# Kernel tuning notes

Measured on AMD Instinct MI355X. Metric: run time of the kernel, lower is better.

## Reference

```python
import jax, jax.numpy as jnp
import numpy as np

N = 12288
F_DIM = 512
H1 = 32
H2 = 16
E_RAND = N * 32  # 393216 random edges; self-loops appended (DGL graph built from adj + I)


def setup_inputs() -> dict:
    key = jax.random.key(0)
    ks = jax.random.split(key, 8)
    feat = jax.random.normal(ks[0], (N, F_DIM), dtype=jnp.float32)
    src_r = jax.random.randint(ks[1], (E_RAND,), 0, N, dtype=jnp.int32)
    dst_r = jax.random.randint(ks[2], (E_RAND,), 0, N, dtype=jnp.int32)
    loop = jnp.arange(N, dtype=jnp.int32)
    src = jnp.concatenate([src_r, loop])  # [E_RAND + N]
    dst = jnp.concatenate([dst_r, loop])
    s1 = 1.0 / np.sqrt(F_DIM)
    s2 = 1.0 / np.sqrt(H1)
    W1 = jax.random.normal(ks[3], (F_DIM, H1), dtype=jnp.float32) * s1
    W2 = jax.random.normal(ks[4], (H1, H2), dtype=jnp.float32) * s2
    W3 = jax.random.normal(ks[5], (H1, H2), dtype=jnp.float32) * s2
    b1 = jnp.zeros((H1,), jnp.float32)
    b2 = jnp.zeros((H2,), jnp.float32)
    b3 = jnp.zeros((H2,), jnp.float32)
    return {"feat": feat, "src": src, "dst": dst,
            "W1": W1, "b1": b1, "W2": W2, "b2": b2, "W3": W3, "b3": b3}


def _norms(src, dst):
    ones = jnp.ones(src.shape[0], jnp.float32)
    deg_out = jax.ops.segment_sum(ones, src, num_segments=N)
    deg_in = jax.ops.segment_sum(ones, dst, num_segments=N)
    inv_sqrt_out = jnp.where(deg_out > 0, jax.lax.rsqrt(jnp.maximum(deg_out, 1.0)), 0.0)
    inv_sqrt_in = jnp.where(deg_in > 0, jax.lax.rsqrt(jnp.maximum(deg_in, 1.0)), 0.0)
    return inv_sqrt_out, inv_sqrt_in


def _graph_conv(x, src, dst, n_src, n_dst, W, b):
    # DGL GraphConv, norm='both': D_in^{-1/2} * A_agg( D_out^{-1/2} * x ) @ W + b
    # (project first when in_dim > out_dim is math-equivalent; do agg-then-W here)
    xn = x * n_src[:, None]
    msg = xn[src]  # gather along edges  [E, d]
    agg = jax.ops.segment_sum(msg, dst, num_segments=N)  # scatter-add SpMM
    h = agg * n_dst[:, None]
    return h @ W + b


def reference(feat, src, dst, W1, b1, W2, b2, W3, b3):
    n_src, n_dst = _norms(src, dst)
    h1 = jax.nn.relu(_graph_conv(feat, src, dst, n_src, n_dst, W1, b1))
    mu = _graph_conv(h1, src, dst, n_src, n_dst, W2, b2)
    logvar = _graph_conv(h1, src, dst, n_src, n_dst, W3, b3)
    # eval-mode reparameterize -> z = mu; InnerProductDecoder with identity act
    z = mu
    adj_rec = z @ z.T  # [N, N] logits
    return adj_rec, mu, logvar
```

## Files before the change

kernel.cpp:

```cpp
#include <hip/hip_runtime.h>
#include <cstddef>

#define NN 12288
#define FD 512
#define H1 32
#define H2 16

typedef float floatx4 __attribute__((ext_vector_type(4)));
typedef float floatx2 __attribute__((ext_vector_type(2)));

__global__ __launch_bounds__(256) void k_gemm1(const float* __restrict__ feat,
                                               const float* __restrict__ W1,
                                               float* __restrict__ P,
                                               int* __restrict__ degz) {
    int gz = blockIdx.x * 256 + threadIdx.x;
    if (gz < 2 * NN) degz[gz] = 0;

    __shared__ float Wlds[FD * H1];
    int tid = threadIdx.x;
    for (int t = tid; t < FD * H1 / 4; t += 256) {
        ((float4*)Wlds)[t] = ((const float4*)W1)[t];
    }
    __syncthreads();

    int row = blockIdx.x * 64 + (tid >> 2);
    int cg  = (tid & 3) * 8;
    float acc[8] = {};
    const float4* f4 = (const float4*)(feat + (size_t)row * FD);
#pragma unroll 4
    for (int k4 = 0; k4 < FD / 4; ++k4) {
        float4 f = f4[k4];
        const float* w = &Wlds[(k4 * 4) * H1 + cg];
#pragma unroll
        for (int j = 0; j < 8; ++j) {
            acc[j] += f.x * w[j] + f.y * w[H1 + j] + f.z * w[2 * H1 + j] + f.w * w[3 * H1 + j];
        }
    }
#pragma unroll
    for (int j = 0; j < 8; ++j) P[(size_t)row * H1 + cg + j] = acc[j];
}

__global__ void k_degree(const int* __restrict__ src, const int* __restrict__ dst,
                         int* __restrict__ deg_out, int* __restrict__ deg_in, int E) {
    int e = blockIdx.x * 256 + threadIdx.x;
    if (e < E) {
        atomicAdd(&deg_out[src[e]], 1);
        atomicAdd(&deg_in[dst[e]], 1);
    }
}

__global__ __launch_bounds__(1024) void k_scan(int* __restrict__ deg_out_cnt,
                                               const int* __restrict__ deg_in,
                                               int* __restrict__ row_ptr,
                                               float* __restrict__ n_src,
                                               float* __restrict__ n_dst) {
    __shared__ int wsum[16];
    int tid = threadIdx.x;
    const int CH = NN / 1024;
    int base = tid * CH;
    int v[CH];
#pragma unroll
    for (int t = 0; t < CH; ++t) v[t] = deg_in[base + t];
    int s = 0;
#pragma unroll
    for (int t = 0; t < CH; ++t) { int x = v[t]; v[t] = s; s += x; }
    int lane = tid & 63;
    int incl = s;
#pragma unroll
    for (int off = 1; off < 64; off <<= 1) {
        int up = __shfl_up(incl, off);
        if (lane >= off) incl += up;
    }
    int wid = tid >> 6;
    if (lane == 63) wsum[wid] = incl;
    __syncthreads();
    if (tid == 0) {
        int a = 0;
        for (int w = 0; w < 16; ++w) { int x = wsum[w]; wsum[w] = a; a += x; }
    }
    __syncthreads();
    int excl = incl - s + wsum[wid];
#pragma unroll
    for (int t = 0; t < CH; ++t) row_ptr[base + t] = excl + v[t];
    if (tid == 1023) row_ptr[NN] = excl + s;

#pragma unroll
    for (int t = 0; t < CH; ++t) {
        int i = base + t;
        n_src[i] = rsqrtf((float)deg_out_cnt[i]);
        n_dst[i] = rsqrtf((float)deg_in[i]);
        deg_out_cnt[i] = 0;
    }
}

__global__ void k_scatter(const int* __restrict__ src, const int* __restrict__ dst,
                          const int* __restrict__ row_ptr, int* __restrict__ cnt,
                          int* __restrict__ sorted_src, int E) {
    int e = blockIdx.x * 256 + threadIdx.x;
    if (e < E) {
        int d = dst[e];
        int pos = row_ptr[d] + atomicAdd(&cnt[d], 1);
        sorted_src[pos] = src[e];
    }
}

__global__ __launch_bounds__(256) void k_agg1(const int* __restrict__ row_ptr,
                                              const int* __restrict__ sorted_src,
                                              const float* __restrict__ P,
                                              const float* __restrict__ n_src,
                                              const float* __restrict__ n_dst,
                                              const float* __restrict__ b1,
                                              float* __restrict__ h1s) {
    int r = blockIdx.x * 8 + (threadIdx.x >> 5);
    int j = threadIdx.x & 31;
    int beg = row_ptr[r], end = row_ptr[r + 1];
    float s = 0.0f;
    int e = beg;
    for (; e + 3 < end; e += 4) {
        int s0 = sorted_src[e], s1 = sorted_src[e + 1];
        int s2 = sorted_src[e + 2], s3 = sorted_src[e + 3];
        float w0 = n_src[s0], w1 = n_src[s1], w2 = n_src[s2], w3 = n_src[s3];
        s += w0 * P[(size_t)s0 * H1 + j] + w1 * P[(size_t)s1 * H1 + j]
           + w2 * P[(size_t)s2 * H1 + j] + w3 * P[(size_t)s3 * H1 + j];
    }
    for (; e < end; ++e) {
        int s0 = sorted_src[e];
        s += n_src[s0] * P[(size_t)s0 * H1 + j];
    }
    float h = fmaxf(s * n_dst[r] + b1[j], 0.0f);
    h1s[(size_t)r * H1 + j] = h * n_src[r];
}

__global__ __launch_bounds__(256) void k_agg2(const int* __restrict__ row_ptr,
                                              const int* __restrict__ sorted_src,
                                              const float* __restrict__ h1s,
                                              const float* __restrict__ n_dst,
                                              const float* __restrict__ W2, const float* __restrict__ b2,
                                              const float* __restrict__ W3, const float* __restrict__ b3,
                                              float* __restrict__ mu, float* __restrict__ lv) {
    __shared__ float W2l[H1 * H2], W3l[H1 * H2];
    __shared__ float S[8][H1];
    int tid = threadIdx.x;
    for (int t = tid; t < H1 * H2; t += 256) { W2l[t] = W2[t]; W3l[t] = W3[t]; }

    int r0 = blockIdx.x * 8;
    int rl = tid >> 5, j = tid & 31;
    int r = r0 + rl;
    int beg = row_ptr[r], end = row_ptr[r + 1];
    float s = 0.0f;
    int e = beg;
    for (; e + 3 < end; e += 4) {
        int s0 = sorted_src[e], s1 = sorted_src[e + 1];
        int s2 = sorted_src[e + 2], s3 = sorted_src[e + 3];
        s += h1s[(size_t)s0 * H1 + j] + h1s[(size_t)s1 * H1 + j]
           + h1s[(size_t)s2 * H1 + j] + h1s[(size_t)s3 * H1 + j];
    }
    for (; e < end; ++e) s += h1s[(size_t)sorted_src[e] * H1 + j];
    S[rl][j] = s * n_dst[r];
    __syncthreads();

    int rr = tid >> 5;
    int c = tid & 15;
    bool is_lv = (tid & 16) != 0;
    const float* W = is_lv ? W3l : W2l;
    float acc = is_lv ? b3[c] : b2[c];
#pragma unroll
    for (int k = 0; k < H1; ++k) acc += S[rr][k] * W[k * H2 + c];
    float* o = is_lv ? lv : mu;
    o[(size_t)(r0 + rr) * H2 + c] = acc;
}

#define TILE 128
__global__ __launch_bounds__(256) void k_adj(const float* __restrict__ mu, float* __restrict__ out) {
    __shared__ float Alt[H2][TILE];
    __shared__ float Blt[H2][TILE];
    int tid = threadIdx.x;
    int i0 = blockIdx.y * TILE;
    int j0 = blockIdx.x * TILE;

    {
        int row = tid >> 1;
        int h8  = (tid & 1) * 8;
        float4 a0 = *(const float4*)&mu[(size_t)(i0 + row) * H2 + h8];
        float4 a1 = *(const float4*)&mu[(size_t)(i0 + row) * H2 + h8 + 4];
        Alt[h8 + 0][row] = a0.x; Alt[h8 + 1][row] = a0.y; Alt[h8 + 2][row] = a0.z; Alt[h8 + 3][row] = a0.w;
        Alt[h8 + 4][row] = a1.x; Alt[h8 + 5][row] = a1.y; Alt[h8 + 6][row] = a1.z; Alt[h8 + 7][row] = a1.w;
        float4 b0 = *(const float4*)&mu[(size_t)(j0 + row) * H2 + h8];
        float4 b1 = *(const float4*)&mu[(size_t)(j0 + row) * H2 + h8 + 4];
        Blt[h8 + 0][row] = b0.x; Blt[h8 + 1][row] = b0.y; Blt[h8 + 2][row] = b0.z; Blt[h8 + 3][row] = b0.w;
        Blt[h8 + 4][row] = b1.x; Blt[h8 + 5][row] = b1.y; Blt[h8 + 6][row] = b1.z; Blt[h8 + 7][row] = b1.w;
    }
    __syncthreads();

    int tx = tid & 15;
    int ty = tid >> 4;
    floatx2 acc2[8][4] = {};
#pragma unroll 2
    for (int k = 0; k < H2; ++k) {
        floatx4 a0 = *(const floatx4*)&Alt[k][ty * 8];
        floatx4 a1 = *(const floatx4*)&Alt[k][ty * 8 + 4];
        floatx4 b0 = *(const floatx4*)&Blt[k][tx * 8];
        floatx4 b1 = *(const floatx4*)&Blt[k][tx * 8 + 4];
        float a[8] = {a0.x, a0.y, a0.z, a0.w, a1.x, a1.y, a1.z, a1.w};
        floatx2 bp[4];
        bp[0] = (floatx2){b0.x, b0.y}; bp[1] = (floatx2){b0.z, b0.w};
        bp[2] = (floatx2){b1.x, b1.y}; bp[3] = (floatx2){b1.z, b1.w};
#pragma unroll
        for (int ii = 0; ii < 8; ++ii) {
            floatx2 av = (floatx2){a[ii], a[ii]};
#pragma unroll
            for (int jp = 0; jp < 4; ++jp)
                acc2[ii][jp] = __builtin_elementwise_fma(av, bp[jp], acc2[ii][jp]);
        }
    }

#pragma unroll
    for (int ii = 0; ii < 8; ++ii) {
        size_t row = (size_t)(i0 + ty * 8 + ii);
        float4 v0 = make_float4(acc2[ii][0].x, acc2[ii][0].y, acc2[ii][1].x, acc2[ii][1].y);
        float4 v1 = make_float4(acc2[ii][2].x, acc2[ii][2].y, acc2[ii][3].x, acc2[ii][3].y);
        *(float4*)&out[row * NN + j0 + tx * 8 + 0] = v0;
        *(float4*)&out[row * NN + j0 + tx * 8 + 4] = v1;
    }
}

extern "C" void kernel_launch(void* const* d_in, const int* in_sizes, int n_in,
                              void* d_out, int out_size, void* d_ws, size_t ws_size,
                              hipStream_t stream) {
    const float* feat = (const float*)d_in[0];
    const int*   src  = (const int*)d_in[1];
    const int*   dst  = (const int*)d_in[2];
    const float* W1   = (const float*)d_in[3];
    const float* b1   = (const float*)d_in[4];
    const float* W2   = (const float*)d_in[5];
    const float* b2   = (const float*)d_in[6];
    const float* W3   = (const float*)d_in[7];
    const float* b3   = (const float*)d_in[8];
    int E = in_sizes[1];

    int* iws = (int*)d_ws;
    int* deg_out_cnt = iws;
    int* deg_in      = iws + NN;
    int* row_ptr     = iws + 2 * NN;
    int* sorted_src  = iws + 3 * NN + 64;
    float* fws   = (float*)(iws + 3 * NN + 64 + E);
    float* n_src = fws;
    float* n_dst = fws + NN;
    float* P     = fws + 2 * NN;
    float* h1s   = fws + 2 * NN + NN * H1;

    float* adj = (float*)d_out;
    float* mu  = adj + (size_t)NN * NN;
    float* lv  = mu + (size_t)NN * H2;

    int eb = (E + 255) / 256;
    k_gemm1<<<NN / 64, 256, 0, stream>>>(feat, W1, P, deg_out_cnt);
    k_degree<<<eb, 256, 0, stream>>>(src, dst, deg_out_cnt, deg_in, E);
    k_scan<<<1, 1024, 0, stream>>>(deg_out_cnt, deg_in, row_ptr, n_src, n_dst);
    k_scatter<<<eb, 256, 0, stream>>>(src, dst, row_ptr, deg_out_cnt, sorted_src, E);
    k_agg1<<<NN / 8, 256, 0, stream>>>(row_ptr, sorted_src, P, n_src, n_dst, b1, h1s);
    k_agg2<<<NN / 8, 256, 0, stream>>>(row_ptr, sorted_src, h1s, n_dst, W2, b2, W3, b3, mu, lv);

    dim3 grid(NN / TILE, NN / TILE);
    k_adj<<<grid, 256, 0, stream>>>(mu, adj);
}
```

Before: 250.4 us.

## Vectorize edge and scan kernels, split aggregation accumulators, add k_adj occupancy hint

```diff
diff --git a/kernel.cpp b/kernel.cpp
--- a/kernel.cpp
+++ b/kernel.cpp
@@ -42,10 +42,21 @@
 
 __global__ void k_degree(const int* __restrict__ src, const int* __restrict__ dst,
                          int* __restrict__ deg_out, int* __restrict__ deg_in, int E) {
-    int e = blockIdx.x * 256 + threadIdx.x;
-    if (e < E) {
-        atomicAdd(&deg_out[src[e]], 1);
-        atomicAdd(&deg_in[dst[e]], 1);
+    int t = blockIdx.x * 256 + threadIdx.x;
+    int E4 = E >> 2;
+    if (t < E4) {
+        int4 s = ((const int4*)src)[t];
+        int4 d = ((const int4*)dst)[t];
+        atomicAdd(&deg_out[s.x], 1); atomicAdd(&deg_out[s.y], 1);
+        atomicAdd(&deg_out[s.z], 1); atomicAdd(&deg_out[s.w], 1);
+        atomicAdd(&deg_in[d.x], 1); atomicAdd(&deg_in[d.y], 1);
+        atomicAdd(&deg_in[d.z], 1); atomicAdd(&deg_in[d.w], 1);
+    }
+    if (t == 0) {
+        for (int e = E4 * 4; e < E; ++e) {
+            atomicAdd(&deg_out[src[e]], 1);
+            atomicAdd(&deg_in[dst[e]], 1);
+        }
     }
 }
 
@@ -58,9 +69,11 @@
     int tid = threadIdx.x;
     const int CH = NN / 1024;
     int base = tid * CH;
-    int v[CH];
-#pragma unroll
-    for (int t = 0; t < CH; ++t) v[t] = deg_in[base + t];
+    int4 va = ((const int4*)deg_in)[tid * 3 + 0];
+    int4 vb = ((const int4*)deg_in)[tid * 3 + 1];
+    int4 vc = ((const int4*)deg_in)[tid * 3 + 2];
+    int v[CH] = {va.x, va.y, va.z, va.w, vb.x, vb.y, vb.z, vb.w, vc.x, vc.y, vc.z, vc.w};
+    int d_in[CH] = {va.x, va.y, va.z, va.w, vb.x, vb.y, vb.z, vb.w, vc.x, vc.y, vc.z, vc.w};
     int s = 0;
 #pragma unroll
     for (int t = 0; t < CH; ++t) { int x = v[t]; v[t] = s; s += x; }
@@ -80,27 +93,52 @@
     }
     __syncthreads();
     int excl = incl - s + wsum[wid];
-#pragma unroll
-    for (int t = 0; t < CH; ++t) row_ptr[base + t] = excl + v[t];
+    {
+        int4 r0 = make_int4(excl + v[0], excl + v[1], excl + v[2], excl + v[3]);
+        int4 r1 = make_int4(excl + v[4], excl + v[5], excl + v[6], excl + v[7]);
+        int4 r2 = make_int4(excl + v[8], excl + v[9], excl + v[10], excl + v[11]);
+        ((int4*)row_ptr)[tid * 3 + 0] = r0;
+        ((int4*)row_ptr)[tid * 3 + 1] = r1;
+        ((int4*)row_ptr)[tid * 3 + 2] = r2;
+    }
     if (tid == 1023) row_ptr[NN] = excl + s;
 
+    int4 da = ((const int4*)deg_out_cnt)[tid * 3 + 0];
+    int4 db = ((const int4*)deg_out_cnt)[tid * 3 + 1];
+    int4 dc = ((const int4*)deg_out_cnt)[tid * 3 + 2];
+    int d_out[CH] = {da.x, da.y, da.z, da.w, db.x, db.y, db.z, db.w, dc.x, dc.y, dc.z, dc.w};
+    float ns[CH], nd[CH];
 #pragma unroll
     for (int t = 0; t < CH; ++t) {
-        int i = base + t;
-        n_src[i] = rsqrtf((float)deg_out_cnt[i]);
-        n_dst[i] = rsqrtf((float)deg_in[i]);
-        deg_out_cnt[i] = 0;
+        ns[t] = rsqrtf((float)d_out[t]);
+        nd[t] = rsqrtf((float)d_in[t]);
+    }
+#pragma unroll
+    for (int q = 0; q < 3; ++q) {
+        ((float4*)n_src)[tid * 3 + q] = make_float4(ns[4*q], ns[4*q+1], ns[4*q+2], ns[4*q+3]);
+        ((float4*)n_dst)[tid * 3 + q] = make_float4(nd[4*q], nd[4*q+1], nd[4*q+2], nd[4*q+3]);
+        ((int4*)deg_out_cnt)[tid * 3 + q] = make_int4(0, 0, 0, 0);
     }
 }
 
 __global__ void k_scatter(const int* __restrict__ src, const int* __restrict__ dst,
                           const int* __restrict__ row_ptr, int* __restrict__ cnt,
                           int* __restrict__ sorted_src, int E) {
-    int e = blockIdx.x * 256 + threadIdx.x;
-    if (e < E) {
-        int d = dst[e];
-        int pos = row_ptr[d] + atomicAdd(&cnt[d], 1);
-        sorted_src[pos] = src[e];
+    int t = blockIdx.x * 256 + threadIdx.x;
+    int E4 = E >> 2;
+    if (t < E4) {
+        int4 s = ((const int4*)src)[t];
+        int4 d = ((const int4*)dst)[t];
+        sorted_src[row_ptr[d.x] + atomicAdd(&cnt[d.x], 1)] = s.x;
+        sorted_src[row_ptr[d.y] + atomicAdd(&cnt[d.y], 1)] = s.y;
+        sorted_src[row_ptr[d.z] + atomicAdd(&cnt[d.z], 1)] = s.z;
+        sorted_src[row_ptr[d.w] + atomicAdd(&cnt[d.w], 1)] = s.w;
+    }
+    if (t == 0) {
+        for (int e = E4 * 4; e < E; ++e) {
+            int d = dst[e];
+            sorted_src[row_ptr[d] + atomicAdd(&cnt[d], 1)] = src[e];
+        }
     }
 }
 
@@ -114,19 +152,19 @@
     int r = blockIdx.x * 8 + (threadIdx.x >> 5);
     int j = threadIdx.x & 31;
     int beg = row_ptr[r], end = row_ptr[r + 1];
-    float s = 0.0f;
+    float sA = 0.0f, sB = 0.0f;
     int e = beg;
     for (; e + 3 < end; e += 4) {
         int s0 = sorted_src[e], s1 = sorted_src[e + 1];
         int s2 = sorted_src[e + 2], s3 = sorted_src[e + 3];
-        float w0 = n_src[s0], w1 = n_src[s1], w2 = n_src[s2], w3 = n_src[s3];
-        s += w0 * P[(size_t)s0 * H1 + j] + w1 * P[(size_t)s1 * H1 + j]
-           + w2 * P[(size_t)s2 * H1 + j] + w3 * P[(size_t)s3 * H1 + j];
+        sA += n_src[s0] * P[(size_t)s0 * H1 + j] + n_src[s1] * P[(size_t)s1 * H1 + j];
+        sB += n_src[s2] * P[(size_t)s2 * H1 + j] + n_src[s3] * P[(size_t)s3 * H1 + j];
     }
     for (; e < end; ++e) {
         int s0 = sorted_src[e];
-        s += n_src[s0] * P[(size_t)s0 * H1 + j];
-    }
+        sA += n_src[s0] * P[(size_t)s0 * H1 + j];
+    }
+    float s = sA + sB;
     float h = fmaxf(s * n_dst[r] + b1[j], 0.0f);
     h1s[(size_t)r * H1 + j] = h * n_src[r];
 }
@@ -147,16 +185,16 @@
     int rl = tid >> 5, j = tid & 31;
     int r = r0 + rl;
     int beg = row_ptr[r], end = row_ptr[r + 1];
-    float s = 0.0f;
+    float sA = 0.0f, sB = 0.0f;
     int e = beg;
     for (; e + 3 < end; e += 4) {
         int s0 = sorted_src[e], s1 = sorted_src[e + 1];
         int s2 = sorted_src[e + 2], s3 = sorted_src[e + 3];
-        s += h1s[(size_t)s0 * H1 + j] + h1s[(size_t)s1 * H1 + j]
-           + h1s[(size_t)s2 * H1 + j] + h1s[(size_t)s3 * H1 + j];
-    }
-    for (; e < end; ++e) s += h1s[(size_t)sorted_src[e] * H1 + j];
-    S[rl][j] = s * n_dst[r];
+        sA += h1s[(size_t)s0 * H1 + j] + h1s[(size_t)s1 * H1 + j];
+        sB += h1s[(size_t)s2 * H1 + j] + h1s[(size_t)s3 * H1 + j];
+    }
+    for (; e < end; ++e) sA += h1s[(size_t)sorted_src[e] * H1 + j];
+    S[rl][j] = (sA + sB) * n_dst[r];
     __syncthreads();
 
     int rr = tid >> 5;
@@ -171,7 +209,7 @@
 }
 
 #define TILE 128
-__global__ __launch_bounds__(256) void k_adj(const float* __restrict__ mu, float* __restrict__ out) {
+__global__ __launch_bounds__(256, 2) void k_adj(const float* __restrict__ mu, float* __restrict__ out) {
     __shared__ float Alt[H2][TILE];
     __shared__ float Blt[H2][TILE];
     int tid = threadIdx.x;
@@ -253,11 +291,11 @@
     float* mu  = adj + (size_t)NN * NN;
     float* lv  = mu + (size_t)NN * H2;
 
-    int eb = (E + 255) / 256;
+    int eb4 = ((E >> 2) + 255) / 256;
     k_gemm1<<<NN / 64, 256, 0, stream>>>(feat, W1, P, deg_out_cnt);
-    k_degree<<<eb, 256, 0, stream>>>(src, dst, deg_out_cnt, deg_in, E);
+    k_degree<<<eb4, 256, 0, stream>>>(src, dst, deg_out_cnt, deg_in, E);
     k_scan<<<1, 1024, 0, stream>>>(deg_out_cnt, deg_in, row_ptr, n_src, n_dst);
-    k_scatter<<<eb, 256, 0, stream>>>(src, dst, row_ptr, deg_out_cnt, sorted_src, E);
+    k_scatter<<<eb4, 256, 0, stream>>>(src, dst, row_ptr, deg_out_cnt, sorted_src, E);
     k_agg1<<<NN / 8, 256, 0, stream>>>(row_ptr, sorted_src, P, n_src, n_dst, b1, h1s);
     k_agg2<<<NN / 8, 256, 0, stream>>>(row_ptr, sorted_src, h1s, n_dst, W2, b2, W3, b3, mu, lv);
 
```

New measurement: 253.3 us. Within noise of the previous version (+1.2%).
